# Optimization experiments

Hardware: AMD Instinct MI355X
Metric: run time of the kernel (lower is better)

## Reference

```python
import jax, jax.numpy as jnp
import numpy as np

INF = 100000000.0
TOPK = 13
ALPHA = 1
BETA = 6


def box_cxcywh_to_xyxy(b):
    cx, cy, w, h = jnp.split(b, 4, axis=-1)
    return jnp.concatenate([cx - 0.5 * w, cy - 0.5 * h, cx + 0.5 * w, cy + 0.5 * h], axis=-1)


def generalized_box_iou(boxes1, boxes2):
    # boxes1: [N,4] xyxy, boxes2: [G,4] xyxy -> [N,G]
    area1 = (boxes1[:, 2] - boxes1[:, 0]) * (boxes1[:, 3] - boxes1[:, 1])
    area2 = (boxes2[:, 2] - boxes2[:, 0]) * (boxes2[:, 3] - boxes2[:, 1])
    lt = jnp.maximum(boxes1[:, None, :2], boxes2[None, :, :2])
    rb = jnp.minimum(boxes1[:, None, 2:], boxes2[None, :, 2:])
    wh = jnp.clip(rb - lt, 0.0)
    inter = wh[..., 0] * wh[..., 1]
    union = area1[:, None] + area2[None, :] - inter
    iou = inter / union
    lt_e = jnp.minimum(boxes1[:, None, :2], boxes2[None, :, :2])
    rb_e = jnp.maximum(boxes1[:, None, 2:], boxes2[None, :, 2:])
    wh_e = jnp.clip(rb_e - lt_e, 0.0)
    area_e = wh_e[..., 0] * wh_e[..., 1]
    return iou - (area_e - union) / area_e


def _assign_one(cls_logits, bbox_pred, gt_boxes, gt_labels):
    # cls_logits [N,C], bbox_pred [N,4] cxcywh, gt_boxes [G,4] cxcywh, gt_labels [G]
    N = bbox_pred.shape[0]
    G = gt_boxes.shape[0]
    scores = jax.nn.sigmoid(cls_logits)
    overlaps = -generalized_box_iou(box_cxcywh_to_xyxy(bbox_pred), box_cxcywh_to_xyxy(gt_boxes))  # [N,G]
    bbox_scores = scores[:, gt_labels]                       # [N,G] gather per-gt class score
    alignment = bbox_scores ** ALPHA * overlaps ** BETA      # [N,G]
    # per-gt topk over queries
    cand_metrics, cand_idxs = jax.lax.top_k(alignment.T, TOPK)  # [G,K]
    is_pos = cand_metrics > 0
    vals = jnp.take_along_axis(overlaps.T, cand_idxs, axis=1)   # [G,K]
    rows = jnp.broadcast_to(jnp.arange(G)[:, None], (G, TOPK))
    cols = jnp.where(is_pos, cand_idxs, N)  # out-of-bounds col -> dropped
    oinf = jnp.full((G, N), -INF, dtype=overlaps.dtype)
    oinf = oinf.at[rows, cols].set(vals, mode='drop')
    max_overlaps = oinf.max(axis=0)     # [N]
    argmax_overlaps = oinf.argmax(axis=0)
    pos = max_overlaps != -INF
    assigned_gt_inds = jnp.where(pos, argmax_overlaps + 1, 0)
    assign_metrics = jnp.where(pos, alignment[jnp.arange(N), argmax_overlaps], 0.0)
    assigned_labels = jnp.where(pos, gt_labels[argmax_overlaps], -1)
    return assigned_gt_inds, assigned_labels, assign_metrics


def setup_inputs() -> dict:
    key = jax.random.key(0)
    k1, k2, k3, k4 = jax.random.split(key, 4)
    bs, N, C, G = 16, 4000, 80, 300
    return {
        'pred_logits': jax.random.normal(k1, (bs, N, C), dtype=jnp.float32),
        'pred_boxes': jax.random.uniform(k2, (bs, N, 4), dtype=jnp.float32, minval=0.05, maxval=0.95),
        'gt_boxes': jax.random.uniform(k3, (bs, G, 4), dtype=jnp.float32, minval=0.05, maxval=0.95),
        'gt_labels': jax.random.randint(k4, (bs, G), 0, C),
    }


def reference(pred_logits, pred_boxes, gt_boxes, gt_labels):
    # Fixed-shape equivalent of matched_list: assigned_gt_inds[b,q] == 0 means
    # background; k>0 means query q matched to gt k-1 (same semantics as the
    # (valid_query_idx, valid_assigned_gt_inds) pairs in the torch code).
    return jax.vmap(_assign_one)(pred_logits, pred_boxes, gt_boxes, gt_labels)
```

## Files before the change

### kernel.cpp

```cpp
#include <hip/hip_runtime.h>

#define NPRED 4000
#define NGT   300
#define NCLS  80
#define TOPKK 13
#define NCHUNK 63

typedef unsigned long long u64;

__device__ __forceinline__ float frcp(float x) { return __builtin_amdgcn_rcpf(x); }
__device__ __forceinline__ float fexp(float x) {
    return __builtin_amdgcn_exp2f(x * 1.44269504088896341f);
}

__device__ __forceinline__ float neg_giou_x(float4 p, float pa, float gx1, float gy1,
                                            float gx2, float gy2, float garea) {
    float whx = fmaxf(fminf(p.z, gx2) - fmaxf(p.x, gx1), 0.0f);
    float why = fmaxf(fminf(p.w, gy2) - fmaxf(p.y, gy1), 0.0f);
    float inter = whx * why;
    float uni = pa + garea - inter;
    float iou = inter * frcp(uni);
    float wex = fmaxf(p.z, gx2) - fminf(p.x, gx1);
    float wey = fmaxf(p.w, gy2) - fminf(p.y, gy1);
    float area_e = wex * wey;
    return (area_e - uni) * frcp(area_e) - iou;
}

__device__ __forceinline__ float4 to_xyxy(float4 pb) {
    return make_float4(pb.x - 0.5f * pb.z, pb.y - 0.5f * pb.w,
                       pb.x + 0.5f * pb.z, pb.y + 0.5f * pb.w);
}

__device__ __forceinline__ float sigmoid_fast(float x) {
    return frcp(1.0f + fexp(-x));
}

__device__ __forceinline__ float pow6(float x) {
    float x2 = x * x;
    float x4 = x2 * x2;
    return x2 * x4;
}

__device__ __forceinline__ unsigned ord_float(float f) {
    unsigned u = __float_as_uint(f);
    return u ^ ((unsigned)(((int)u) >> 31) | 0x80000000u);
}

__global__ void init_keys(u64* keys, int n) {
    int i = blockIdx.x * blockDim.x + threadIdx.x;
    if (i < n) keys[i] = 0ULL;
}

__global__ __launch_bounds__(256) void sig_transpose(const float* __restrict__ logits,
                                                     const float4* __restrict__ pboxes,
                                                     float* __restrict__ st,
                                                     float4* __restrict__ pxyxy,
                                                     float* __restrict__ parea,
                                                     u64* __restrict__ keys,
                                                     int total_keys) {
    const int tid = threadIdx.x;
    const int gid = blockIdx.x * 256 + tid;
    if (gid < total_keys) keys[gid] = 0ULL;

    const int b = blockIdx.x / NCHUNK;
    const int n0 = (blockIdx.x % NCHUNK) * 64;
    const int nval = (NPRED - n0 < 64) ? (NPRED - n0) : 64;

    if (tid < 64 && tid < nval) {
        float4 p = to_xyxy(pboxes[(size_t)b * NPRED + n0 + tid]);
        pxyxy[(size_t)b * NPRED + n0 + tid] = p;
        parea[(size_t)b * NPRED + n0 + tid] = (p.z - p.x) * (p.w - p.y);
    }

    __shared__ float tile[NCLS][64 + 1];

    const float4* src = (const float4*)(logits + ((size_t)b * NPRED + n0) * NCLS);
    #pragma unroll
    for (int it = 0; it < 5; ++it) {
        int i4 = tid + it * 256;
        int p = i4 / 20;
        int c = i4 * 4 - p * 80;
        if (p < nval) {
            float4 v = src[i4];
            tile[c + 0][p] = sigmoid_fast(v.x);
            tile[c + 1][p] = sigmoid_fast(v.y);
            tile[c + 2][p] = sigmoid_fast(v.z);
            tile[c + 3][p] = sigmoid_fast(v.w);
        }
    }
    __syncthreads();
    float* dstbase = st + (size_t)b * NCLS * NPRED + n0;
    #pragma unroll
    for (int it = 0; it < 5; ++it) {
        int w4 = tid + it * 256;
        int c = w4 >> 4, r4 = (w4 & 15) * 4;
        if (r4 < nval) {
            float4 v = make_float4(tile[c][r4], tile[c][r4 + 1],
                                   tile[c][r4 + 2], tile[c][r4 + 3]);
            *(float4*)(dstbase + (size_t)c * NPRED + r4) = v;
        }
    }
}

template <bool PRE>
__global__ __launch_bounds__(256) void topk_scatter(const float* __restrict__ logits,
                                                    const float* __restrict__ st,
                                                    const float4* __restrict__ pboxes,
                                                    const float4* __restrict__ pxyxy,
                                                    const float* __restrict__ parea,
                                                    const float4* __restrict__ gboxes,
                                                    const int* __restrict__ glabels,
                                                    u64* __restrict__ keys) {
    const int blk = blockIdx.x;
    const int b = blk / NGT;
    const int g = blk - b * NGT;
    const int tid = threadIdx.x;

    __shared__ unsigned s_key[NPRED];
    __shared__ unsigned s_rv[8];
    __shared__ int      s_ri[8];
    __shared__ int      s_win[TOPKK];
    __shared__ unsigned s_winv[TOPKK];

    float4 gb = gboxes[b * NGT + g];
    const int lab = glabels[b * NGT + g];
    const float gx1 = gb.x - 0.5f * gb.z;
    const float gy1 = gb.y - 0.5f * gb.w;
    const float gx2 = gb.x + 0.5f * gb.z;
    const float gy2 = gb.y + 0.5f * gb.w;
    const float garea = (gx2 - gx1) * (gy2 - gy1);

    const float* lg = logits + (size_t)b * NPRED * NCLS + lab;
    const float* srow = st + ((size_t)b * NCLS + lab) * NPRED;
    const float4* pbb = pboxes + (size_t)b * NPRED;
    const float4* pxr = pxyxy + (size_t)b * NPRED;
    const float* par = parea + (size_t)b * NPRED;

    unsigned b1v = 0u; int b1i = 0x7FFFFFFF;
    unsigned b2v = 0u; int b2i = 0x7FFFFFFF;
    #pragma unroll 4
    for (int n = tid; n < NPRED; n += 256) {
        float o, s;
        if (PRE) {
            o = neg_giou_x(pxr[n], par[n], gx1, gy1, gx2, gy2, garea);
            s = srow[n];
        } else {
            float4 p = to_xyxy(pbb[n]);
            o = neg_giou_x(p, (p.z - p.x) * (p.w - p.y), gx1, gy1, gx2, gy2, garea);
            s = sigmoid_fast(lg[(size_t)n * NCLS]);
        }
        unsigned v = ord_float(s * pow6(o));
        s_key[n] = v;
        if (v > b1v)      { b2v = b1v; b2i = b1i; b1v = v; b1i = n; }
        else if (v > b2v) { b2v = v; b2i = n; }
    }

    int nwin = 0;
    for (int k = 0; k < TOPKK; ++k) {
        unsigned rv = b1v; int ri = b1i;
        #pragma unroll
        for (int off = 32; off > 0; off >>= 1) {
            unsigned v2 = __shfl_down(rv, off, 64);
            int      i2 = __shfl_down(ri, off, 64);
            bool take = (v2 > rv) || (v2 == rv && i2 < ri);
            rv = take ? v2 : rv;
            ri = take ? i2 : ri;
        }
        const int buf = (k & 1) * 4;
        if ((tid & 63) == 0) { s_rv[buf + (tid >> 6)] = rv; s_ri[buf + (tid >> 6)] = ri; }
        __syncthreads();
        unsigned wv = s_rv[buf]; int wi = s_ri[buf];
        #pragma unroll
        for (int w = 1; w < 4; ++w) {
            unsigned v2 = s_rv[buf + w]; int i2 = s_ri[buf + w];
            if (v2 > wv || (v2 == wv && i2 < wi)) { wv = v2; wi = i2; }
        }
        if (wv <= 0x80000000u) break;
        if (tid == 0) { s_win[k] = wi; s_winv[k] = wv; }
        nwin = k + 1;
        if (tid == (wi & 255)) {
            s_key[wi] = 0u;
            if (b2v != 0u) {
                b1v = b2v; b1i = b2i; b2v = 0u; b2i = 0x7FFFFFFF;
            } else {
                b1v = 0u; b1i = 0x7FFFFFFF;
                #pragma unroll 4
                for (int n = tid; n < NPRED; n += 256) {
                    unsigned v = s_key[n];
                    if (v > b1v)      { b2v = b1v; b2i = b1i; b1v = v; b1i = n; }
                    else if (v > b2v) { b2v = v; b2i = n; }
                }
            }
        }
    }
    __syncthreads();

    if (tid < nwin) {
        int wi = s_win[tid];
        unsigned av = s_winv[tid];
        unsigned mbits = (av & 0x7FFFFFFFu) >> 16;
        float o;
        if (PRE) {
            o = neg_giou_x(pxr[wi], par[wi], gx1, gy1, gx2, gy2, garea);
        } else {
            float4 p = to_xyxy(pbb[wi]);
            o = neg_giou_x(p, (p.z - p.x) * (p.w - p.y), gx1, gy1, gx2, gy2, garea);
        }
        u64 key = ((u64)ord_float(o) << 32)
                | ((u64)(511u - (unsigned)g) << 23)
                | ((u64)mbits << 7);
        atomicMax(&keys[(size_t)b * NPRED + wi], key);
    }
}

__global__ void finalize(const int* __restrict__ glabels,
                         const u64* __restrict__ keys,
                         float* __restrict__ out, int total) {
    int i = blockIdx.x * blockDim.x + threadIdx.x;
    if (i >= total) return;
    int b = i / NPRED;
    u64 key = keys[i];
    float o0 = 0.0f, o1 = -1.0f, o2 = 0.0f;
    if (key != 0ULL) {
        int g = 511 - (int)((key >> 23) & 0x1FF);
        o0 = (float)(g + 1);
        o1 = (float)glabels[b * NGT + g];
        o2 = __uint_as_float(((unsigned)(key >> 7) & 0xFFFFu) << 16);
    }
    out[i] = o0;
    out[(size_t)total + i] = o1;
    out[(size_t)2 * total + i] = o2;
}

extern "C" void kernel_launch(void* const* d_in, const int* in_sizes, int n_in,
                              void* d_out, int out_size, void* d_ws, size_t ws_size,
                              hipStream_t stream) {
    const float* logits  = (const float*)d_in[0];
    const float4* pboxes = (const float4*)d_in[1];
    const float4* gboxes = (const float4*)d_in[2];
    const int* glabels   = (const int*)d_in[3];

    const int bs = in_sizes[3] / NGT;
    const int total = bs * NPRED;
    char* ws = (char*)d_ws;
    u64* keys    = (u64*)ws;                                  ws += (size_t)total * 8;
    float* st    = (float*)ws;                                ws += (size_t)bs * NCLS * NPRED * 4;
    float4* pxy  = (float4*)ws;                               ws += (size_t)total * 16;
    float* par   = (float*)ws;                                ws += (size_t)total * 4;
    float* out = (float*)d_out;

    const size_t need = (size_t)(ws - (char*)d_ws);
    if (ws_size >= need) {
        sig_transpose<<<bs * NCHUNK, 256, 0, stream>>>(logits, pboxes, st, pxy, par,
                                                       keys, total);
        topk_scatter<true><<<bs * NGT, 256, 0, stream>>>(logits, st, pboxes, pxy, par,
                                                         gboxes, glabels, keys);
    } else {
        init_keys<<<(total + 255) / 256, 256, 0, stream>>>(keys, total);
        topk_scatter<false><<<bs * NGT, 256, 0, stream>>>(logits, st, pboxes, pxy, par,
                                                          gboxes, glabels, keys);
    }
    finalize<<<(total + 255) / 256, 256, 0, stream>>>(glabels, keys, out, total);
}
```

Baseline: 143.4 us.

## Assign one wavefront per gt box and recompute candidates instead of LDS keys

The top-k scatter kernel now gives each ground-truth box a single 64-lane wavefront instead of a 256-thread block. This removes the per-iteration __syncthreads and the cross-wave reduction through shared memory, and drops the 16KB LDS key array. When a lane runs out of cached top-2 candidates, it recomputes the alignment metrics from global memory and skips already-removed entries using a 64-bit bitmask. The precomputed area buffer is also removed and areas are recomputed inline. The trade-offs are 4x more serial work per wave in the scan and possible extra global reloads on refill.

```diff
diff --git a/kernel.cpp b/kernel.cpp
--- a/kernel.cpp
+++ b/kernel.cpp
@@ -13,8 +13,9 @@
     return __builtin_amdgcn_exp2f(x * 1.44269504088896341f);
 }
 
-__device__ __forceinline__ float neg_giou_x(float4 p, float pa, float gx1, float gy1,
+__device__ __forceinline__ float neg_giou_x(float4 p, float gx1, float gy1,
                                             float gx2, float gy2, float garea) {
+    float pa = (p.z - p.x) * (p.w - p.y);
     float whx = fmaxf(fminf(p.z, gx2) - fmaxf(p.x, gx1), 0.0f);
     float why = fmaxf(fminf(p.w, gy2) - fmaxf(p.y, gy1), 0.0f);
     float inter = whx * why;
@@ -55,7 +56,6 @@
                                                      const float4* __restrict__ pboxes,
                                                      float* __restrict__ st,
                                                      float4* __restrict__ pxyxy,
-                                                     float* __restrict__ parea,
                                                      u64* __restrict__ keys,
                                                      int total_keys) {
     const int tid = threadIdx.x;
@@ -67,9 +67,8 @@
     const int nval = (NPRED - n0 < 64) ? (NPRED - n0) : 64;
 
     if (tid < 64 && tid < nval) {
-        float4 p = to_xyxy(pboxes[(size_t)b * NPRED + n0 + tid]);
-        pxyxy[(size_t)b * NPRED + n0 + tid] = p;
-        parea[(size_t)b * NPRED + n0 + tid] = (p.z - p.x) * (p.w - p.y);
+        pxyxy[(size_t)b * NPRED + n0 + tid] =
+            to_xyxy(pboxes[(size_t)b * NPRED + n0 + tid]);
     }
 
     __shared__ float tile[NCLS][64 + 1];
@@ -107,23 +106,18 @@
                                                     const float* __restrict__ st,
                                                     const float4* __restrict__ pboxes,
                                                     const float4* __restrict__ pxyxy,
-                                                    const float* __restrict__ parea,
                                                     const float4* __restrict__ gboxes,
                                                     const int* __restrict__ glabels,
-                                                    u64* __restrict__ keys) {
-    const int blk = blockIdx.x;
-    const int b = blk / NGT;
-    const int g = blk - b * NGT;
-    const int tid = threadIdx.x;
-
-    __shared__ unsigned s_key[NPRED];
-    __shared__ unsigned s_rv[8];
-    __shared__ int      s_ri[8];
-    __shared__ int      s_win[TOPKK];
-    __shared__ unsigned s_winv[TOPKK];
-
-    float4 gb = gboxes[b * NGT + g];
-    const int lab = glabels[b * NGT + g];
+                                                    u64* __restrict__ keys,
+                                                    int ngt_total) {
+    const int gid = (blockIdx.x * 256 + threadIdx.x) >> 6;
+    if (gid >= ngt_total) return;
+    const int b = gid / NGT;
+    const int g = gid - b * NGT;
+    const int lane = threadIdx.x & 63;
+
+    float4 gb = gboxes[gid];
+    const int lab = glabels[gid];
     const float gx1 = gb.x - 0.5f * gb.z;
     const float gy1 = gb.y - 0.5f * gb.w;
     const float gx2 = gb.x + 0.5f * gb.z;
@@ -134,82 +128,71 @@
     const float* srow = st + ((size_t)b * NCLS + lab) * NPRED;
     const float4* pbb = pboxes + (size_t)b * NPRED;
     const float4* pxr = pxyxy + (size_t)b * NPRED;
-    const float* par = parea + (size_t)b * NPRED;
 
     unsigned b1v = 0u; int b1i = 0x7FFFFFFF;
     unsigned b2v = 0u; int b2i = 0x7FFFFFFF;
-    #pragma unroll 4
-    for (int n = tid; n < NPRED; n += 256) {
+    for (int n = lane; n < NPRED; n += 64) {
         float o, s;
         if (PRE) {
-            o = neg_giou_x(pxr[n], par[n], gx1, gy1, gx2, gy2, garea);
+            o = neg_giou_x(pxr[n], gx1, gy1, gx2, gy2, garea);
             s = srow[n];
         } else {
-            float4 p = to_xyxy(pbb[n]);
-            o = neg_giou_x(p, (p.z - p.x) * (p.w - p.y), gx1, gy1, gx2, gy2, garea);
+            o = neg_giou_x(to_xyxy(pbb[n]), gx1, gy1, gx2, gy2, garea);
             s = sigmoid_fast(lg[(size_t)n * NCLS]);
         }
         unsigned v = ord_float(s * pow6(o));
-        s_key[n] = v;
         if (v > b1v)      { b2v = b1v; b2i = b1i; b1v = v; b1i = n; }
         else if (v > b2v) { b2v = v; b2i = n; }
     }
 
-    int nwin = 0;
+    u64 removed = 0ULL;
+    unsigned myv = 0u; int mywin = -1;
     for (int k = 0; k < TOPKK; ++k) {
-        unsigned rv = b1v; int ri = b1i;
+        unsigned wv = b1v; int wi = b1i;
         #pragma unroll
-        for (int off = 32; off > 0; off >>= 1) {
-            unsigned v2 = __shfl_down(rv, off, 64);
-            int      i2 = __shfl_down(ri, off, 64);
-            bool take = (v2 > rv) || (v2 == rv && i2 < ri);
-            rv = take ? v2 : rv;
-            ri = take ? i2 : ri;
-        }
-        const int buf = (k & 1) * 4;
-        if ((tid & 63) == 0) { s_rv[buf + (tid >> 6)] = rv; s_ri[buf + (tid >> 6)] = ri; }
-        __syncthreads();
-        unsigned wv = s_rv[buf]; int wi = s_ri[buf];
-        #pragma unroll
-        for (int w = 1; w < 4; ++w) {
-            unsigned v2 = s_rv[buf + w]; int i2 = s_ri[buf + w];
+        for (int m = 1; m < 64; m <<= 1) {
+            unsigned v2 = __shfl_xor(wv, m, 64);
+            int      i2 = __shfl_xor(wi, m, 64);
             if (v2 > wv || (v2 == wv && i2 < wi)) { wv = v2; wi = i2; }
         }
         if (wv <= 0x80000000u) break;
-        if (tid == 0) { s_win[k] = wi; s_winv[k] = wv; }
-        nwin = k + 1;
-        if (tid == (wi & 255)) {
-            s_key[wi] = 0u;
+        if (lane == k) { mywin = wi; myv = wv; }
+        if (lane == (wi & 63)) {
+            removed |= 1ULL << (wi >> 6);
             if (b2v != 0u) {
                 b1v = b2v; b1i = b2i; b2v = 0u; b2i = 0x7FFFFFFF;
             } else {
                 b1v = 0u; b1i = 0x7FFFFFFF;
-                #pragma unroll 4
-                for (int n = tid; n < NPRED; n += 256) {
-                    unsigned v = s_key[n];
+                for (int n = lane, j = 0; n < NPRED; n += 64, ++j) {
+                    if ((removed >> j) & 1ULL) continue;
+                    float o, s;
+                    if (PRE) {
+                        o = neg_giou_x(pxr[n], gx1, gy1, gx2, gy2, garea);
+                        s = srow[n];
+                    } else {
+                        o = neg_giou_x(to_xyxy(pbb[n]), gx1, gy1, gx2, gy2, garea);
+                        s = sigmoid_fast(lg[(size_t)n * NCLS]);
+                    }
+                    unsigned v = ord_float(s * pow6(o));
                     if (v > b1v)      { b2v = b1v; b2i = b1i; b1v = v; b1i = n; }
                     else if (v > b2v) { b2v = v; b2i = n; }
                 }
             }
         }
     }
-    __syncthreads();
-
-    if (tid < nwin) {
-        int wi = s_win[tid];
-        unsigned av = s_winv[tid];
-        unsigned mbits = (av & 0x7FFFFFFFu) >> 16;
+
+    if (mywin >= 0) {
         float o;
         if (PRE) {
-            o = neg_giou_x(pxr[wi], par[wi], gx1, gy1, gx2, gy2, garea);
+            o = neg_giou_x(pxr[mywin], gx1, gy1, gx2, gy2, garea);
         } else {
-            float4 p = to_xyxy(pbb[wi]);
-            o = neg_giou_x(p, (p.z - p.x) * (p.w - p.y), gx1, gy1, gx2, gy2, garea);
-        }
+            o = neg_giou_x(to_xyxy(pbb[mywin]), gx1, gy1, gx2, gy2, garea);
+        }
+        unsigned mbits = (myv & 0x7FFFFFFFu) >> 16;
         u64 key = ((u64)ord_float(o) << 32)
                 | ((u64)(511u - (unsigned)g) << 23)
                 | ((u64)mbits << 7);
-        atomicMax(&keys[(size_t)b * NPRED + wi], key);
+        atomicMax(&keys[(size_t)b * NPRED + mywin], key);
     }
 }
 
@@ -242,23 +225,24 @@
 
     const int bs = in_sizes[3] / NGT;
     const int total = bs * NPRED;
+    const int ngt_total = bs * NGT;
     char* ws = (char*)d_ws;
-    u64* keys    = (u64*)ws;                                  ws += (size_t)total * 8;
-    float* st    = (float*)ws;                                ws += (size_t)bs * NCLS * NPRED * 4;
-    float4* pxy  = (float4*)ws;                               ws += (size_t)total * 16;
-    float* par   = (float*)ws;                                ws += (size_t)total * 4;
+    u64* keys   = (u64*)ws;                    ws += (size_t)total * 8;
+    float* st   = (float*)ws;                  ws += (size_t)bs * NCLS * NPRED * 4;
+    float4* pxy = (float4*)ws;                 ws += (size_t)total * 16;
     float* out = (float*)d_out;
 
+    const int tblocks = (ngt_total * 64 + 255) / 256;
     const size_t need = (size_t)(ws - (char*)d_ws);
     if (ws_size >= need) {
-        sig_transpose<<<bs * NCHUNK, 256, 0, stream>>>(logits, pboxes, st, pxy, par,
+        sig_transpose<<<bs * NCHUNK, 256, 0, stream>>>(logits, pboxes, st, pxy,
                                                        keys, total);
-        topk_scatter<true><<<bs * NGT, 256, 0, stream>>>(logits, st, pboxes, pxy, par,
-                                                         gboxes, glabels, keys);
+        topk_scatter<true><<<tblocks, 256, 0, stream>>>(logits, st, pboxes, pxy,
+                                                        gboxes, glabels, keys, ngt_total);
     } else {
         init_keys<<<(total + 255) / 256, 256, 0, stream>>>(keys, total);
-        topk_scatter<false><<<bs * NGT, 256, 0, stream>>>(logits, st, pboxes, pxy, par,
-                                                          gboxes, glabels, keys);
+        topk_scatter<false><<<tblocks, 256, 0, stream>>>(logits, st, pboxes, pxy,
+                                                         gboxes, glabels, keys, ngt_total);
     }
     finalize<<<(total + 255) / 256, 256, 0, stream>>>(glabels, keys, out, total);
 }
```

After: 216.3 us. +50.8%, slower.

## Process four contiguous queries per thread, drop area buffer, use float keys

Applied to the files above, without the earlier changes.

Each thread in the top-k kernel now handles four contiguous queries, loading the class-score row as float4 and four box float4s, instead of striding one query at a time. The precomputed prediction-area buffer is removed and the area is recomputed in registers, which saves a global read and write per query. Selection keys are now raw floats instead of order-mapped unsigned values, which removes the conversion. The cost is more registers per thread and strided LDS writes, and the ownership mapping for the rescan changes accordingly.

```diff
diff --git a/kernel.cpp b/kernel.cpp
--- a/kernel.cpp
+++ b/kernel.cpp
@@ -1,9 +1,10 @@
 #include <hip/hip_runtime.h>
 
-#define NPRED 4000
-#define NGT   300
-#define NCLS  80
-#define TOPKK 13
+#define NPRED  4000
+#define NGROUP 1000
+#define NGT    300
+#define NCLS   80
+#define TOPKK  13
 #define NCHUNK 63
 
 typedef unsigned long long u64;
@@ -13,8 +14,9 @@
     return __builtin_amdgcn_exp2f(x * 1.44269504088896341f);
 }
 
-__device__ __forceinline__ float neg_giou_x(float4 p, float pa, float gx1, float gy1,
+__device__ __forceinline__ float neg_giou_x(float4 p, float gx1, float gy1,
                                             float gx2, float gy2, float garea) {
+    float pa  = (p.z - p.x) * (p.w - p.y);
     float whx = fmaxf(fminf(p.z, gx2) - fmaxf(p.x, gx1), 0.0f);
     float why = fmaxf(fminf(p.w, gy2) - fmaxf(p.y, gy1), 0.0f);
     float inter = whx * why;
@@ -55,7 +57,6 @@
                                                      const float4* __restrict__ pboxes,
                                                      float* __restrict__ st,
                                                      float4* __restrict__ pxyxy,
-                                                     float* __restrict__ parea,
                                                      u64* __restrict__ keys,
                                                      int total_keys) {
     const int tid = threadIdx.x;
@@ -67,9 +68,8 @@
     const int nval = (NPRED - n0 < 64) ? (NPRED - n0) : 64;
 
     if (tid < 64 && tid < nval) {
-        float4 p = to_xyxy(pboxes[(size_t)b * NPRED + n0 + tid]);
-        pxyxy[(size_t)b * NPRED + n0 + tid] = p;
-        parea[(size_t)b * NPRED + n0 + tid] = (p.z - p.x) * (p.w - p.y);
+        pxyxy[(size_t)b * NPRED + n0 + tid] =
+            to_xyxy(pboxes[(size_t)b * NPRED + n0 + tid]);
     }
 
     __shared__ float tile[NCLS][64 + 1];
@@ -107,7 +107,6 @@
                                                     const float* __restrict__ st,
                                                     const float4* __restrict__ pboxes,
                                                     const float4* __restrict__ pxyxy,
-                                                    const float* __restrict__ parea,
                                                     const float4* __restrict__ gboxes,
                                                     const int* __restrict__ glabels,
                                                     u64* __restrict__ keys) {
@@ -116,11 +115,11 @@
     const int g = blk - b * NGT;
     const int tid = threadIdx.x;
 
-    __shared__ unsigned s_key[NPRED];
-    __shared__ unsigned s_rv[8];
-    __shared__ int      s_ri[8];
-    __shared__ int      s_win[TOPKK];
-    __shared__ unsigned s_winv[TOPKK];
+    __shared__ float s_key[NPRED];
+    __shared__ float s_rv[8];
+    __shared__ int   s_ri[8];
+    __shared__ int   s_win[TOPKK];
+    __shared__ float s_winv[TOPKK];
 
     float4 gb = gboxes[b * NGT + g];
     const int lab = glabels[b * NGT + g];
@@ -132,36 +131,55 @@
 
     const float* lg = logits + (size_t)b * NPRED * NCLS + lab;
     const float* srow = st + ((size_t)b * NCLS + lab) * NPRED;
+    const float4* srow4 = (const float4*)srow;
     const float4* pbb = pboxes + (size_t)b * NPRED;
     const float4* pxr = pxyxy + (size_t)b * NPRED;
-    const float* par = parea + (size_t)b * NPRED;
-
-    unsigned b1v = 0u; int b1i = 0x7FFFFFFF;
-    unsigned b2v = 0u; int b2i = 0x7FFFFFFF;
-    #pragma unroll 4
-    for (int n = tid; n < NPRED; n += 256) {
-        float o, s;
-        if (PRE) {
-            o = neg_giou_x(pxr[n], par[n], gx1, gy1, gx2, gy2, garea);
-            s = srow[n];
-        } else {
-            float4 p = to_xyxy(pbb[n]);
-            o = neg_giou_x(p, (p.z - p.x) * (p.w - p.y), gx1, gy1, gx2, gy2, garea);
-            s = sigmoid_fast(lg[(size_t)n * NCLS]);
-        }
-        unsigned v = ord_float(s * pow6(o));
-        s_key[n] = v;
-        if (v > b1v)      { b2v = b1v; b2i = b1i; b1v = v; b1i = n; }
-        else if (v > b2v) { b2v = v; b2i = n; }
+
+    float b1v = -1.0f, b2v = -1.0f;
+    int b1i = 0x7FFFFFFF, b2i = 0x7FFFFFFF;
+    #pragma unroll
+    for (int j = 0; j < 4; ++j) {
+        int grp = tid + j * 256;
+        if (grp < NGROUP) {
+            int n0 = grp * 4;
+            float s0, s1, s2, s3;
+            float4 p0, p1, p2, p3;
+            if (PRE) {
+                float4 s4 = srow4[grp];
+                s0 = s4.x; s1 = s4.y; s2 = s4.z; s3 = s4.w;
+                p0 = pxr[n0]; p1 = pxr[n0 + 1]; p2 = pxr[n0 + 2]; p3 = pxr[n0 + 3];
+            } else {
+                s0 = sigmoid_fast(lg[(size_t)(n0 + 0) * NCLS]);
+                s1 = sigmoid_fast(lg[(size_t)(n0 + 1) * NCLS]);
+                s2 = sigmoid_fast(lg[(size_t)(n0 + 2) * NCLS]);
+                s3 = sigmoid_fast(lg[(size_t)(n0 + 3) * NCLS]);
+                p0 = to_xyxy(pbb[n0]);     p1 = to_xyxy(pbb[n0 + 1]);
+                p2 = to_xyxy(pbb[n0 + 2]); p3 = to_xyxy(pbb[n0 + 3]);
+            }
+            float v0 = s0 * pow6(neg_giou_x(p0, gx1, gy1, gx2, gy2, garea));
+            float v1 = s1 * pow6(neg_giou_x(p1, gx1, gy1, gx2, gy2, garea));
+            float v2 = s2 * pow6(neg_giou_x(p2, gx1, gy1, gx2, gy2, garea));
+            float v3 = s3 * pow6(neg_giou_x(p3, gx1, gy1, gx2, gy2, garea));
+            s_key[n0 + 0] = v0; s_key[n0 + 1] = v1;
+            s_key[n0 + 2] = v2; s_key[n0 + 3] = v3;
+            if (v0 > b1v)      { b2v = b1v; b2i = b1i; b1v = v0; b1i = n0; }
+            else if (v0 > b2v) { b2v = v0; b2i = n0; }
+            if (v1 > b1v)      { b2v = b1v; b2i = b1i; b1v = v1; b1i = n0 + 1; }
+            else if (v1 > b2v) { b2v = v1; b2i = n0 + 1; }
+            if (v2 > b1v)      { b2v = b1v; b2i = b1i; b1v = v2; b1i = n0 + 2; }
+            else if (v2 > b2v) { b2v = v2; b2i = n0 + 2; }
+            if (v3 > b1v)      { b2v = b1v; b2i = b1i; b1v = v3; b1i = n0 + 3; }
+            else if (v3 > b2v) { b2v = v3; b2i = n0 + 3; }
+        }
     }
 
     int nwin = 0;
     for (int k = 0; k < TOPKK; ++k) {
-        unsigned rv = b1v; int ri = b1i;
+        float rv = b1v; int ri = b1i;
         #pragma unroll
         for (int off = 32; off > 0; off >>= 1) {
-            unsigned v2 = __shfl_down(rv, off, 64);
-            int      i2 = __shfl_down(ri, off, 64);
+            float v2 = __shfl_down(rv, off, 64);
+            int   i2 = __shfl_down(ri, off, 64);
             bool take = (v2 > rv) || (v2 == rv && i2 < ri);
             rv = take ? v2 : rv;
             ri = take ? i2 : ri;
@@ -169,26 +187,33 @@
         const int buf = (k & 1) * 4;
         if ((tid & 63) == 0) { s_rv[buf + (tid >> 6)] = rv; s_ri[buf + (tid >> 6)] = ri; }
         __syncthreads();
-        unsigned wv = s_rv[buf]; int wi = s_ri[buf];
+        float wv = s_rv[buf]; int wi = s_ri[buf];
         #pragma unroll
         for (int w = 1; w < 4; ++w) {
-            unsigned v2 = s_rv[buf + w]; int i2 = s_ri[buf + w];
+            float v2 = s_rv[buf + w]; int i2 = s_ri[buf + w];
             if (v2 > wv || (v2 == wv && i2 < wi)) { wv = v2; wi = i2; }
         }
-        if (wv <= 0x80000000u) break;
+        if (!(wv > 0.0f)) break;
         if (tid == 0) { s_win[k] = wi; s_winv[k] = wv; }
         nwin = k + 1;
-        if (tid == (wi & 255)) {
-            s_key[wi] = 0u;
-            if (b2v != 0u) {
-                b1v = b2v; b1i = b2i; b2v = 0u; b2i = 0x7FFFFFFF;
+        if (tid == ((wi >> 2) & 255)) {
+            s_key[wi] = -1.0f;
+            if (b2i != 0x7FFFFFFF) {
+                b1v = b2v; b1i = b2i; b2v = -1.0f; b2i = 0x7FFFFFFF;
             } else {
-                b1v = 0u; b1i = 0x7FFFFFFF;
-                #pragma unroll 4
-                for (int n = tid; n < NPRED; n += 256) {
-                    unsigned v = s_key[n];
-                    if (v > b1v)      { b2v = b1v; b2i = b1i; b1v = v; b1i = n; }
-                    else if (v > b2v) { b2v = v; b2i = n; }
+                b1v = -1.0f; b1i = 0x7FFFFFFF;
+                #pragma unroll
+                for (int jj = 0; jj < 4; ++jj) {
+                    int grp = tid + jj * 256;
+                    if (grp >= NGROUP) continue;
+                    int n0 = grp * 4;
+                    #pragma unroll
+                    for (int sb = 0; sb < 4; ++sb) {
+                        int n = n0 + sb;
+                        float v = s_key[n];
+                        if (v > b1v)      { b2v = b1v; b2i = b1i; b1v = v; b1i = n; }
+                        else if (v > b2v) { b2v = v; b2i = n; }
+                    }
                 }
             }
         }
@@ -197,15 +222,13 @@
 
     if (tid < nwin) {
         int wi = s_win[tid];
-        unsigned av = s_winv[tid];
-        unsigned mbits = (av & 0x7FFFFFFFu) >> 16;
         float o;
         if (PRE) {
-            o = neg_giou_x(pxr[wi], par[wi], gx1, gy1, gx2, gy2, garea);
+            o = neg_giou_x(pxr[wi], gx1, gy1, gx2, gy2, garea);
         } else {
-            float4 p = to_xyxy(pbb[wi]);
-            o = neg_giou_x(p, (p.z - p.x) * (p.w - p.y), gx1, gy1, gx2, gy2, garea);
-        }
+            o = neg_giou_x(to_xyxy(pbb[wi]), gx1, gy1, gx2, gy2, garea);
+        }
+        unsigned mbits = __float_as_uint(s_winv[tid]) >> 16;
         u64 key = ((u64)ord_float(o) << 32)
                 | ((u64)(511u - (unsigned)g) << 23)
                 | ((u64)mbits << 7);
@@ -243,21 +266,20 @@
     const int bs = in_sizes[3] / NGT;
     const int total = bs * NPRED;
     char* ws = (char*)d_ws;
-    u64* keys    = (u64*)ws;                                  ws += (size_t)total * 8;
-    float* st    = (float*)ws;                                ws += (size_t)bs * NCLS * NPRED * 4;
-    float4* pxy  = (float4*)ws;                               ws += (size_t)total * 16;
-    float* par   = (float*)ws;                                ws += (size_t)total * 4;
+    u64* keys   = (u64*)ws;                    ws += (size_t)total * 8;
+    float* st   = (float*)ws;                  ws += (size_t)bs * NCLS * NPRED * 4;
+    float4* pxy = (float4*)ws;                 ws += (size_t)total * 16;
     float* out = (float*)d_out;
 
     const size_t need = (size_t)(ws - (char*)d_ws);
     if (ws_size >= need) {
-        sig_transpose<<<bs * NCHUNK, 256, 0, stream>>>(logits, pboxes, st, pxy, par,
+        sig_transpose<<<bs * NCHUNK, 256, 0, stream>>>(logits, pboxes, st, pxy,
                                                        keys, total);
-        topk_scatter<true><<<bs * NGT, 256, 0, stream>>>(logits, st, pboxes, pxy, par,
+        topk_scatter<true><<<bs * NGT, 256, 0, stream>>>(logits, st, pboxes, pxy,
                                                          gboxes, glabels, keys);
     } else {
         init_keys<<<(total + 255) / 256, 256, 0, stream>>>(keys, total);
-        topk_scatter<false><<<bs * NGT, 256, 0, stream>>>(logits, st, pboxes, pxy, par,
+        topk_scatter<false><<<bs * NGT, 256, 0, stream>>>(logits, st, pboxes, pxy,
                                                           gboxes, glabels, keys);
     }
     finalize<<<(total + 255) / 256, 256, 0, stream>>>(glabels, keys, out, total);
```

Result: faster. 137.7 us (-4.0%).
